# Optimization experiments

Measured on AMD Instinct MI355X. Metric: run time of the kernel, lower is better.

Reference implementation:

```python
import jax, jax.numpy as jnp
import numpy as np

B, L, H, NH = 4, 2048, 2048, 16
HD = H // NH  # head_dim = 128


def setup_inputs() -> dict:
    key = jax.random.key(0)
    ks = jax.random.split(key, 5)
    x = jax.random.normal(ks[0], (B, L, H), dtype=jnp.float32)
    Wqkv = jax.random.normal(ks[1], (H, 3 * H), dtype=jnp.float32) * (1.0 / np.sqrt(H))
    bqkv = jnp.zeros((3 * H,), dtype=jnp.float32)
    Wfc2 = jax.random.normal(ks[2], (H, H), dtype=jnp.float32) * (1.0 / np.sqrt(H))
    bfc2 = jnp.zeros((H,), dtype=jnp.float32)
    # RoPE tables over the FULL hidden dim (as in the torch module)
    inv_freq = 1.0 / (10000.0 ** (jnp.arange(0, H, 2, dtype=jnp.float32) / H))  # [H/2]
    t = jnp.arange(L, dtype=jnp.float32)
    freqs = jnp.outer(t, inv_freq)  # [L, H/2]
    return {"x": x, "Wqkv": Wqkv, "bqkv": bqkv, "Wfc2": Wfc2, "bfc2": bfc2,
            "cos": jnp.cos(freqs), "sin": jnp.sin(freqs)}


def _apply_rotary(u, cos, sin):
    # u: [b, l, H]; rotate halves over full hidden dim
    l = u.shape[1]
    d = u.shape[-1] // 2
    u1, u2 = u[..., :d], u[..., d:]
    c, s = cos[:l], sin[:l]  # [l, d] broadcast over batch
    return jnp.concatenate([u1 * c + u2 * s, -u1 * s + u2 * c], axis=-1)


def reference(x, Wqkv, bqkv, Wfc2, bfc2, cos, sin):
    b, l, _ = x.shape
    qkv = x @ Wqkv + bqkv  # [b, l, 3H]
    q, k, v = jnp.split(qkv, 3, axis=-1)
    q = _apply_rotary(q, cos, sin)
    k = _apply_rotary(k, cos, sin)
    # NOTE: heads are the FASTEST axis in the original view(b, l, head_dim, heads)
    def to_heads(u):
        return jnp.transpose(u.reshape(b, l, HD, NH), (0, 3, 1, 2))  # [b, h, l, d]
    q, k, v = to_heads(q), to_heads(k), to_heads(v)
    scale = 1.0 / np.sqrt(HD)
    scores = jnp.einsum('bhqd,bhkd->bhqk', q, k) * scale
    causal = jnp.tril(jnp.ones((l, l), dtype=bool))
    scores = jnp.where(causal, scores, jnp.finfo(scores.dtype).min)
    p = jax.nn.softmax(scores, axis=-1)
    y = jnp.einsum('bhqk,bhkd->bhqd', p, v)
    y = jnp.transpose(y, (0, 2, 1, 3)).reshape(b, l, H)  # [b, l, h*d]
    return jax.nn.silu(y @ Wfc2 + bfc2)
```

## Files before the change

### kernel.cpp

```cpp
#include <hip/hip_runtime.h>
#include <hip/hip_bf16.h>
#include <cstdint>
#include <cstddef>


typedef __attribute__((ext_vector_type(4))) float f32x4;
typedef __attribute__((ext_vector_type(8))) short bf16x8;
typedef __hip_bfloat16 bf16;

#define ASYNC16(lds, g)                                                                  \
  __builtin_amdgcn_global_load_lds((const __attribute__((address_space(1))) void*)(g),   \
                                   (__attribute__((address_space(3))) void*)(lds), 16, 0, 0)

__device__ __forceinline__ float b2f(bf16 v) { return __bfloat162float(v); }
__device__ __forceinline__ bf16 f2b(float v) { return __float2bfloat16(v); }
__device__ __forceinline__ short f2bs(float f) {
  bf16 h = __float2bfloat16(f);
  return __builtin_bit_cast(short, h);
}
__device__ __forceinline__ bf16x8 pack8(f32x4 a, f32x4 b) {
  bf16x8 r;
#pragma unroll
  for (int t = 0; t < 4; ++t) r[t] = f2bs(a[t]);
#pragma unroll
  for (int t = 0; t < 4; ++t) r[4 + t] = f2bs(b[t]);
  return r;
}

template <int CTRL>
__device__ __forceinline__ float dpp_bfly_max(float x) {
  int xi = __builtin_bit_cast(int, x);
  int yi = __builtin_amdgcn_update_dpp(xi, xi, CTRL, 0xF, 0xF, false);
  return fmaxf(x, __builtin_bit_cast(float, yi));
}
template <int CTRL>
__device__ __forceinline__ float dpp_bfly_add(float x) {
  int xi = __builtin_bit_cast(int, x);
  int yi = __builtin_amdgcn_update_dpp(xi, xi, CTRL, 0xF, 0xF, false);
  return x + __builtin_bit_cast(float, yi);
}

__global__ void conv_bf16(const float* __restrict__ src, bf16* __restrict__ dst) {
  size_t i = ((size_t)blockIdx.x * 256 + threadIdx.x) * 8;
  f32x4 a0 = *(const f32x4*)(src + i);
  f32x4 a1 = *(const f32x4*)(src + i + 4);
  *(bf16x8*)(dst + i) = pack8(a0, a1);
}

__global__ void transpose_conv(const float* __restrict__ src, bf16* __restrict__ dst,
                               int R, int C, int perm) {
  __shared__ float tile[32][33];
  int bx = blockIdx.x * 32, by = blockIdx.y * 32;
  int tx = threadIdx.x, ty = threadIdx.y;
  for (int i = ty; i < 32; i += 8) tile[i][tx] = src[(size_t)(by + i) * C + bx + tx];
  __syncthreads();
  for (int i = ty; i < 32; i += 8) {
    int c = bx + i;
    if (perm) {
      int cc = c & 2047;
      c = (c & ~2047) | (((cc & 15) << 7) | (cc >> 4));
    }
    dst[(size_t)c * R + by + tx] = f2b(tile[tx][i]);
  }
}

__global__ __launch_bounds__(256) void gemm_qkv(const bf16* __restrict__ A,
                                                const bf16* __restrict__ Bt,
                                                const float* __restrict__ biasf,
                                                bf16* __restrict__ Qg, bf16* __restrict__ Kg,
                                                bf16* __restrict__ Vg) {
  __shared__ alignas(16) bf16 smem[2 * 128 * 64];
  bf16* As = smem;
  bf16* Bs = smem + 128 * 64;
  const int K_ = 2048;
  int tid = threadIdx.x, lane = tid & 63, w = tid >> 6;
  int lr = lane & 15, hi = lane >> 4;
  int wm = (w >> 1) * 64, wn = (w & 1) * 64;
  int m0 = blockIdx.y * 128, n0 = blockIdx.x * 128;
  f32x4 acc[4][4];
#pragma unroll
  for (int im = 0; im < 4; ++im)
#pragma unroll
    for (int in = 0; in < 4; ++in) acc[im][in] = (f32x4){0.f, 0.f, 0.f, 0.f};

  for (int k0 = 0; k0 < K_; k0 += 64) {
    __syncthreads();
#pragma unroll
    for (int i = 0; i < 4; ++i) {
      int c = tid + 256 * i;
      int r = c >> 3, j = c & 7, jg = j ^ (r & 7);
      ASYNC16((char*)As + c * 16, (const char*)(A + (size_t)(m0 + r) * K_ + k0 + jg * 8));
    }
#pragma unroll
    for (int i = 0; i < 4; ++i) {
      int c = tid + 256 * i;
      int r = c >> 3, j = c & 7, jg = j ^ (r & 7);
      ASYNC16((char*)Bs + c * 16, (const char*)(Bt + (size_t)(n0 + r) * K_ + k0 + jg * 8));
    }
    __syncthreads();

#pragma unroll
    for (int ks = 0; ks < 2; ++ks) {
      bf16x8 afr[4], bfr[4];
#pragma unroll
      for (int im = 0; im < 4; ++im) {
        int r = wm + 16 * im + lr;
        afr[im] = *(const bf16x8*)((const char*)As + r * 128 + (((ks * 4 + hi) ^ (r & 7)) * 16));
      }
#pragma unroll
      for (int in = 0; in < 4; ++in) {
        int r = wn + 16 * in + lr;
        bfr[in] = *(const bf16x8*)((const char*)Bs + r * 128 + (((ks * 4 + hi) ^ (r & 7)) * 16));
      }
#pragma unroll
      for (int im = 0; im < 4; ++im)
#pragma unroll
        for (int in = 0; in < 4; ++in)
          acc[im][in] =
              __builtin_amdgcn_mfma_f32_16x16x32_bf16(afr[im], bfr[in], acc[im][in], 0, 0, 0);
    }
  }

  int which = n0 >> 11;
  int h = (n0 >> 7) & 15;
  int bq = m0 >> 11;
  int l_base = m0 & 2047;
  int bh = bq * 16 + h;
  float bv[4];
#pragma unroll
  for (int in = 0; in < 4; ++in)
    bv[in] = biasf[(which << 11) + ((wn + 16 * in + lr) << 4) + h];

  if (which < 2) {
    bf16* __restrict__ G = (which == 0) ? Qg : Kg;
#pragma unroll
    for (int im = 0; im < 4; ++im) {
#pragma unroll
      for (int in = 0; in < 4; ++in) {
        int d = wn + 16 * in + lr;
#pragma unroll
        for (int j = 0; j < 4; ++j) {
          int l = l_base + wm + 16 * im + 4 * hi + j;
          G[((size_t)bh * 2048 + l) * 128 + d] = f2b(acc[im][in][j] + bv[in]);
        }
      }
    }
  } else {
    __syncthreads();
#pragma unroll
    for (int im = 0; im < 4; ++im)
#pragma unroll
      for (int in = 0; in < 4; ++in) {
        int d = wn + 16 * in + lr;
#pragma unroll
        for (int j = 0; j < 4; ++j) {
          int l = wm + 16 * im + 4 * hi + j;
          int slot = (l >> 3) ^ (d & 15);
          smem[d * 128 + slot * 8 + (l & 7)] = f2b(acc[im][in][j] + bv[in]);
        }
      }
    __syncthreads();
#pragma unroll
    for (int s = 0; s < 8; ++s) {
      int d = (tid >> 4) + 16 * s;
      int lc = tid & 15;
      int slot = lc ^ (d & 15);
      bf16x8 v = *(const bf16x8*)(smem + d * 128 + slot * 8);
      *(bf16x8*)(Vg + ((size_t)bh * 128 + d) * 2048 + l_base + lc * 8) = v;
    }
  }
}

__global__ __launch_bounds__(256) void gemm_fc2(const bf16* __restrict__ A,
                                                const bf16* __restrict__ Bt,
                                                const float* __restrict__ biasf,
                                                float* __restrict__ Out) {
  __shared__ alignas(16) bf16 As[128 * 64];
  __shared__ alignas(16) bf16 Bs[128 * 64];
  const int K_ = 2048;
  int tid = threadIdx.x, lane = tid & 63, w = tid >> 6;
  int lr = lane & 15, hi = lane >> 4;
  int wm = (w >> 1) * 64, wn = (w & 1) * 64;
  int m0 = blockIdx.y * 128, n0 = blockIdx.x * 128;
  f32x4 acc[4][4];
#pragma unroll
  for (int im = 0; im < 4; ++im)
#pragma unroll
    for (int in = 0; in < 4; ++in) acc[im][in] = (f32x4){0.f, 0.f, 0.f, 0.f};

  for (int k0 = 0; k0 < K_; k0 += 64) {
    __syncthreads();
#pragma unroll
    for (int i = 0; i < 4; ++i) {
      int c = tid + 256 * i;
      int r = c >> 3, j = c & 7, jg = j ^ (r & 7);
      ASYNC16((char*)As + c * 16, (const char*)(A + (size_t)(m0 + r) * K_ + k0 + jg * 8));
    }
#pragma unroll
    for (int i = 0; i < 4; ++i) {
      int c = tid + 256 * i;
      int r = c >> 3, j = c & 7, jg = j ^ (r & 7);
      ASYNC16((char*)Bs + c * 16, (const char*)(Bt + (size_t)(n0 + r) * K_ + k0 + jg * 8));
    }
    __syncthreads();
#pragma unroll
    for (int ks = 0; ks < 2; ++ks) {
      bf16x8 afr[4], bfr[4];
#pragma unroll
      for (int im = 0; im < 4; ++im) {
        int r = wm + 16 * im + lr;
        afr[im] = *(const bf16x8*)((const char*)As + r * 128 + (((ks * 4 + hi) ^ (r & 7)) * 16));
      }
#pragma unroll
      for (int in = 0; in < 4; ++in) {
        int r = wn + 16 * in + lr;
        bfr[in] = *(const bf16x8*)((const char*)Bs + r * 128 + (((ks * 4 + hi) ^ (r & 7)) * 16));
      }
#pragma unroll
      for (int im = 0; im < 4; ++im)
#pragma unroll
        for (int in = 0; in < 4; ++in)
          acc[im][in] =
              __builtin_amdgcn_mfma_f32_16x16x32_bf16(afr[im], bfr[in], acc[im][in], 0, 0, 0);
    }
  }

#pragma unroll
  for (int im = 0; im < 4; ++im) {
#pragma unroll
    for (int in = 0; in < 4; ++in) {
      int c = n0 + wn + 16 * in + lr;
      float bv = biasf[c];
#pragma unroll
      for (int j = 0; j < 4; ++j) {
        int m = m0 + wm + 16 * im + 4 * hi + j;
        float z = acc[im][in][j] + bv;
        Out[(size_t)m * 2048 + c] = z / (1.f + __expf(-z));
      }
    }
  }
}

__global__ void rotary_kernel(bf16* __restrict__ Qg, bf16* __restrict__ Kg,
                              const float* __restrict__ cosp, const float* __restrict__ sinp) {
  int idx = blockIdx.x * 256 + threadIdx.x;
  int d = idx & 63;
  int l = (idx >> 6) & 2047;
  int bh = idx >> 17;
  int h = bh & 15;
  size_t base = ((size_t)bh * 2048 + l) * 128;
  int ang = l * 1024 + d * 16 + h;
  float c = cosp[ang], s = sinp[ang];
  float q1 = b2f(Qg[base + d]), q2 = b2f(Qg[base + d + 64]);
  Qg[base + d] = f2b(q1 * c + q2 * s);
  Qg[base + d + 64] = f2b(-q1 * s + q2 * c);
  float k1 = b2f(Kg[base + d]), k2 = b2f(Kg[base + d + 64]);
  Kg[base + d] = f2b(k1 * c + k2 * s);
  Kg[base + d + 64] = f2b(-k1 * s + k2 * c);
}

__global__ __launch_bounds__(512) void flash_kernel(const bf16* __restrict__ Qg,
                                                    const bf16* __restrict__ Kg,
                                                    const bf16* __restrict__ Vg,
                                                    bf16* __restrict__ Y) {
  __shared__ alignas(16) bf16 Ks[64 * 128];
  __shared__ alignas(16) bf16 Vt[128 * 64];
  __shared__ alignas(16) bf16 Ps[8 * 16 * 72];
  int tid = threadIdx.x, lane = tid & 63, w = tid >> 6;
  int lr = lane & 15, hi = lane >> 4;
  int it = 15 - (int)blockIdx.x;
  int bh = blockIdx.y;
  int b = bh >> 4, h = bh & 15;
  int q0 = it * 128;
  int qb = q0 + 16 * w;
  const bf16* Qb = Qg + (size_t)bh * 2048 * 128;
  const bf16* Kb = Kg + (size_t)bh * 2048 * 128;
  const bf16* Vb = Vg + (size_t)bh * 128 * 2048;
  const float NEG = -1.0e30f;

  bf16x8 qf[4];
#pragma unroll
  for (int ks = 0; ks < 4; ++ks)
    qf[ks] = *(const bf16x8*)(Qb + (size_t)(qb + lr) * 128 + (ks * 4 + hi) * 8);

  bf16x8 kreg[2], vreg[2];
#pragma unroll
  for (int i = 0; i < 2; ++i) {
    int c = tid + 512 * i;
    int rk = c >> 4, jk = (c & 15) ^ (rk & 7);
    kreg[i] = *(const bf16x8*)(Kb + (size_t)rk * 128 + jk * 8);
    int rv = c >> 3, jv = (c & 7) ^ (rv & 7);
    vreg[i] = *(const bf16x8*)(Vb + (size_t)rv * 2048 + jv * 8);
  }

  f32x4 o[8];
#pragma unroll
  for (int i = 0; i < 8; ++i) o[i] = (f32x4){0.f, 0.f, 0.f, 0.f};
  float m_i[4], l_i[4];
#pragma unroll
  for (int j = 0; j < 4; ++j) { m_i[j] = NEG; l_i[j] = 0.f; }
  const float scale = 0.08838834764831845f;

  int jt_max = 2 * it + 1;
  for (int jt = 0; jt <= jt_max; ++jt) {
    int k0 = jt * 64;
    __syncthreads();
#pragma unroll
    for (int i = 0; i < 2; ++i) {
      int c = tid + 512 * i;
      *(bf16x8*)((char*)Ks + c * 16) = kreg[i];
      *(bf16x8*)((char*)Vt + c * 16) = vreg[i];
    }
    __syncthreads();

    if (jt < jt_max) {
      int k0n = k0 + 64;
#pragma unroll
      for (int i = 0; i < 2; ++i) {
        int c = tid + 512 * i;
        int rk = c >> 4, jk = (c & 15) ^ (rk & 7);
        kreg[i] = *(const bf16x8*)(Kb + (size_t)(k0n + rk) * 128 + jk * 8);
        int rv = c >> 3, jv = (c & 7) ^ (rv & 7);
        vreg[i] = *(const bf16x8*)(Vb + (size_t)rv * 2048 + k0n + jv * 8);
      }
    }

    if (k0 > qb + 15) continue;

    f32x4 sacc[4];
#pragma unroll
    for (int in = 0; in < 4; ++in) sacc[in] = (f32x4){0.f, 0.f, 0.f, 0.f};
#pragma unroll
    for (int ks = 0; ks < 4; ++ks) {
#pragma unroll
      for (int in = 0; in < 4; ++in) {
        int br = 16 * in + lr;
        bf16x8 bb =
            *(const bf16x8*)((const char*)Ks + br * 256 + (((ks * 4 + hi) ^ (br & 7)) * 16));
        sacc[in] = __builtin_amdgcn_mfma_f32_16x16x32_bf16(qf[ks], bb, sacc[in], 0, 0, 0);
      }
    }

    bool needmask = (k0 + 63 > qb);
    float mxr[4], alpha[4], rsum[4];
#pragma unroll
    for (int j = 0; j < 4; ++j) {
      float mx = NEG;
#pragma unroll
      for (int in = 0; in < 4; ++in) {
        float s = sacc[in][j] * scale;
        if (needmask) {
          int qg_ = qb + 4 * hi + j;
          int kg_ = k0 + 16 * in + lr;
          if (kg_ > qg_) s = NEG;
        }
        sacc[in][j] = s;
        mx = fmaxf(mx, s);
      }
      mxr[j] = mx;
    }
#pragma unroll
    for (int j = 0; j < 4; ++j) mxr[j] = dpp_bfly_max<0xB1>(mxr[j]);
#pragma unroll
    for (int j = 0; j < 4; ++j) mxr[j] = dpp_bfly_max<0x4E>(mxr[j]);
#pragma unroll
    for (int j = 0; j < 4; ++j) mxr[j] = dpp_bfly_max<0x141>(mxr[j]);
#pragma unroll
    for (int j = 0; j < 4; ++j) mxr[j] = dpp_bfly_max<0x140>(mxr[j]);

#pragma unroll
    for (int j = 0; j < 4; ++j) {
      float mnew = fmaxf(m_i[j], mxr[j]);
      alpha[j] = __expf(m_i[j] - mnew);
      m_i[j] = mnew;
      float r = 0.f;
#pragma unroll
      for (int in = 0; in < 4; ++in) {
        float p = __expf(sacc[in][j] - mnew);
        sacc[in][j] = p;
        r += p;
      }
      rsum[j] = r;
    }
#pragma unroll
    for (int j = 0; j < 4; ++j) rsum[j] = dpp_bfly_add<0xB1>(rsum[j]);
#pragma unroll
    for (int j = 0; j < 4; ++j) rsum[j] = dpp_bfly_add<0x4E>(rsum[j]);
#pragma unroll
    for (int j = 0; j < 4; ++j) rsum[j] = dpp_bfly_add<0x141>(rsum[j]);
#pragma unroll
    for (int j = 0; j < 4; ++j) rsum[j] = dpp_bfly_add<0x140>(rsum[j]);

#pragma unroll
    for (int j = 0; j < 4; ++j) {
      l_i[j] = alpha[j] * l_i[j] + rsum[j];
#pragma unroll
      for (int inp = 0; inp < 8; ++inp) o[inp][j] *= alpha[j];
    }

#pragma unroll
    for (int j = 0; j < 4; ++j)
#pragma unroll
      for (int in = 0; in < 4; ++in)
        Ps[w * 1152 + (4 * hi + j) * 72 + 16 * in + lr] = f2b(sacc[in][j]);
    asm volatile("s_waitcnt lgkmcnt(0)" ::: "memory");

#pragma unroll
    for (int ko = 0; ko < 2; ++ko) {
      bf16x8 a = *(const bf16x8*)((const char*)Ps + (w * 1152 + lr * 72 + ko * 32 + hi * 8) * 2);
#pragma unroll
      for (int inp = 0; inp < 8; ++inp) {
        int br = 16 * inp + lr;
        bf16x8 bb =
            *(const bf16x8*)((const char*)Vt + br * 128 + (((ko * 4 + hi) ^ (br & 7)) * 16));
        o[inp] = __builtin_amdgcn_mfma_f32_16x16x32_bf16(a, bb, o[inp], 0, 0, 0);
      }
    }
  }

#pragma unroll
  for (int j = 0; j < 4; ++j) {
    int qg_ = qb + 4 * hi + j;
    float inv = 1.f / l_i[j];
    size_t rowb = ((size_t)(b * 2048 + qg_)) * 2048 + h * 128;
#pragma unroll
    for (int inp = 0; inp < 8; ++inp) {
      int dd = 16 * inp + lr;
      Y[rowb + dd] = f2b(o[inp][j] * inv);
    }
  }
}

extern "C" void kernel_launch(void* const* d_in, const int* in_sizes, int n_in,
                              void* d_out, int out_size, void* d_ws, size_t ws_size,
                              hipStream_t stream) {
  const float* x    = (const float*)d_in[0];
  const float* Wqkv = (const float*)d_in[1];
  const float* bqkv = (const float*)d_in[2];
  const float* Wfc2 = (const float*)d_in[3];
  const float* bfc2 = (const float*)d_in[4];
  const float* cosp = (const float*)d_in[5];
  const float* sinp = (const float*)d_in[6];
  float* out = (float*)d_out;

  bf16* ws = (bf16*)d_ws;
  bf16* Yg    = ws;
  bf16* WqkvT = ws;
  bf16* Qg    = ws + 16777216;
  bf16* Wfc2T = ws + 16777216;
  bf16* Kg    = ws + 33554432;
  bf16* Vg    = ws + 50331648;
  bf16* xb    = (bf16*)d_out;

  conv_bf16<<<8192, 256, 0, stream>>>(x, xb);
  transpose_conv<<<dim3(192, 64), dim3(32, 8), 0, stream>>>(Wqkv, WqkvT, 2048, 6144, 1);
  gemm_qkv<<<dim3(48, 64), 256, 0, stream>>>(xb, WqkvT, bqkv, Qg, Kg, Vg);
  rotary_kernel<<<32768, 256, 0, stream>>>(Qg, Kg, cosp, sinp);
  flash_kernel<<<dim3(16, 64), 512, 0, stream>>>(Qg, Kg, Vg, Yg);
  transpose_conv<<<dim3(64, 64), dim3(32, 8), 0, stream>>>(Wfc2, Wfc2T, 2048, 2048, 0);
  gemm_fc2<<<dim3(16, 64), 256, 0, stream>>>(Yg, Wfc2T, bfc2, out);
}
```

Baseline: 801.3 us.

## Fuse rotary into QKV epilogue and flash Q load; add lazy softmax rescale

Drops the standalone rotary kernel. RoPE on K now runs in the QKV GEMM epilogue through an LDS-staged, swizzled row layout, and RoPE on Q is applied to the Q fragments in registers when the flash kernel loads them. This removes a full read-modify-write pass over Q and K. The flash kernel also skips the running-max update and the output rescale when every row's new max stays within 8 of the old one (a wave-wide vote), and the row-sum reductions are reordered after the P stores. The cost is extra cos/sin gathers inside both kernels and somewhat larger unnormalised exponentials when the rescale is skipped.

```diff
diff --git a/kernel.cpp b/kernel.cpp
--- a/kernel.cpp
+++ b/kernel.cpp
@@ -17,6 +17,9 @@
 __device__ __forceinline__ short f2bs(float f) {
   bf16 h = __float2bfloat16(f);
   return __builtin_bit_cast(short, h);
+}
+__device__ __forceinline__ float s2f(short s) {
+  return __bfloat162float(__builtin_bit_cast(bf16, s));
 }
 __device__ __forceinline__ bf16x8 pack8(f32x4 a, f32x4 b) {
   bf16x8 r;
@@ -67,6 +70,8 @@
 __global__ __launch_bounds__(256) void gemm_qkv(const bf16* __restrict__ A,
                                                 const bf16* __restrict__ Bt,
                                                 const float* __restrict__ biasf,
+                                                const float* __restrict__ cosp,
+                                                const float* __restrict__ sinp,
                                                 bf16* __restrict__ Qg, bf16* __restrict__ Kg,
                                                 bf16* __restrict__ Vg) {
   __shared__ alignas(16) bf16 smem[2 * 128 * 64];
@@ -131,8 +136,7 @@
   for (int in = 0; in < 4; ++in)
     bv[in] = biasf[(which << 11) + ((wn + 16 * in + lr) << 4) + h];
 
-  if (which < 2) {
-    bf16* __restrict__ G = (which == 0) ? Qg : Kg;
+  if (which == 0) {
 #pragma unroll
     for (int im = 0; im < 4; ++im) {
 #pragma unroll
@@ -141,9 +145,46 @@
 #pragma unroll
         for (int j = 0; j < 4; ++j) {
           int l = l_base + wm + 16 * im + 4 * hi + j;
-          G[((size_t)bh * 2048 + l) * 128 + d] = f2b(acc[im][in][j] + bv[in]);
+          Qg[((size_t)bh * 2048 + l) * 128 + d] = f2b(acc[im][in][j] + bv[in]);
         }
       }
+    }
+  } else if (which == 1) {
+    __syncthreads();
+#pragma unroll
+    for (int im = 0; im < 4; ++im)
+#pragma unroll
+      for (int in = 0; in < 4; ++in) {
+        int d = wn + 16 * in + lr;
+#pragma unroll
+        for (int j = 0; j < 4; ++j) {
+          int lw = wm + 16 * im + 4 * hi + j;
+          smem[lw * 128 + (((d >> 3) ^ (lw & 15)) << 3) + (d & 7)] =
+              f2b(acc[im][in][j] + bv[in]);
+        }
+      }
+    __syncthreads();
+#pragma unroll
+    for (int t = 0; t < 4; ++t) {
+      int g = tid + 256 * t;
+      int lw = g >> 3, c = g & 7;
+      bf16x8 v1 = *(const bf16x8*)(smem + lw * 128 + ((c ^ (lw & 15)) << 3));
+      bf16x8 v2 = *(const bf16x8*)(smem + lw * 128 + (((c + 8) ^ (lw & 15)) << 3));
+      int l = l_base + lw;
+      size_t abase = (size_t)l * 1024 + h;
+      bf16x8 r1, r2;
+#pragma unroll
+      for (int e = 0; e < 8; ++e) {
+        int dd = c * 8 + e;
+        float cv = cosp[abase + dd * 16];
+        float sv = sinp[abase + dd * 16];
+        float k1 = s2f(v1[e]), k2 = s2f(v2[e]);
+        r1[e] = f2bs(k1 * cv + k2 * sv);
+        r2[e] = f2bs(-k1 * sv + k2 * cv);
+      }
+      bf16* Kr = Kg + ((size_t)bh * 2048 + l) * 128;
+      *(bf16x8*)(Kr + c * 8) = r1;
+      *(bf16x8*)(Kr + c * 8 + 64) = r2;
     }
   } else {
     __syncthreads();
@@ -241,27 +282,11 @@
   }
 }
 
-__global__ void rotary_kernel(bf16* __restrict__ Qg, bf16* __restrict__ Kg,
-                              const float* __restrict__ cosp, const float* __restrict__ sinp) {
-  int idx = blockIdx.x * 256 + threadIdx.x;
-  int d = idx & 63;
-  int l = (idx >> 6) & 2047;
-  int bh = idx >> 17;
-  int h = bh & 15;
-  size_t base = ((size_t)bh * 2048 + l) * 128;
-  int ang = l * 1024 + d * 16 + h;
-  float c = cosp[ang], s = sinp[ang];
-  float q1 = b2f(Qg[base + d]), q2 = b2f(Qg[base + d + 64]);
-  Qg[base + d] = f2b(q1 * c + q2 * s);
-  Qg[base + d + 64] = f2b(-q1 * s + q2 * c);
-  float k1 = b2f(Kg[base + d]), k2 = b2f(Kg[base + d + 64]);
-  Kg[base + d] = f2b(k1 * c + k2 * s);
-  Kg[base + d + 64] = f2b(-k1 * s + k2 * c);
-}
-
 __global__ __launch_bounds__(512) void flash_kernel(const bf16* __restrict__ Qg,
                                                     const bf16* __restrict__ Kg,
                                                     const bf16* __restrict__ Vg,
+                                                    const float* __restrict__ cosp,
+                                                    const float* __restrict__ sinp,
                                                     bf16* __restrict__ Y) {
   __shared__ alignas(16) bf16 Ks[64 * 128];
   __shared__ alignas(16) bf16 Vt[128 * 64];
@@ -282,6 +307,20 @@
 #pragma unroll
   for (int ks = 0; ks < 4; ++ks)
     qf[ks] = *(const bf16x8*)(Qb + (size_t)(qb + lr) * 128 + (ks * 4 + hi) * 8);
+  {
+    size_t arow = (size_t)(qb + lr) * 1024 + h;
+#pragma unroll
+    for (int ks = 0; ks < 2; ++ks)
+#pragma unroll
+      for (int e = 0; e < 8; ++e) {
+        int dd = 32 * ks + 8 * hi + e;
+        float cv = cosp[arow + dd * 16];
+        float sv = sinp[arow + dd * 16];
+        float q1 = s2f(qf[ks][e]), q2 = s2f(qf[ks + 2][e]);
+        qf[ks][e] = f2bs(q1 * cv + q2 * sv);
+        qf[ks + 2][e] = f2bs(-q1 * sv + q2 * cv);
+      }
+  }
 
   bf16x8 kreg[2], vreg[2];
 #pragma unroll
@@ -342,7 +381,7 @@
     }
 
     bool needmask = (k0 + 63 > qb);
-    float mxr[4], alpha[4], rsum[4];
+    float mxr[4];
 #pragma unroll
     for (int j = 0; j < 4; ++j) {
       float mx = NEG;
@@ -368,41 +407,56 @@
 #pragma unroll
     for (int j = 0; j < 4; ++j) mxr[j] = dpp_bfly_max<0x140>(mxr[j]);
 
+    int okc = 1;
+#pragma unroll
+    for (int j = 0; j < 4; ++j) okc &= (mxr[j] <= m_i[j] + 8.f) ? 1 : 0;
+    bool skip = __all(okc);
+    float mnew[4];
+#pragma unroll
+    for (int j = 0; j < 4; ++j) mnew[j] = skip ? m_i[j] : fmaxf(m_i[j], mxr[j]);
+
+    float rsum[4];
 #pragma unroll
     for (int j = 0; j < 4; ++j) {
-      float mnew = fmaxf(m_i[j], mxr[j]);
-      alpha[j] = __expf(m_i[j] - mnew);
-      m_i[j] = mnew;
       float r = 0.f;
 #pragma unroll
       for (int in = 0; in < 4; ++in) {
-        float p = __expf(sacc[in][j] - mnew);
+        float p = __expf(sacc[in][j] - mnew[j]);
         sacc[in][j] = p;
         r += p;
       }
       rsum[j] = r;
     }
-#pragma unroll
-    for (int j = 0; j < 4; ++j) rsum[j] = dpp_bfly_add<0xB1>(rsum[j]);
-#pragma unroll
-    for (int j = 0; j < 4; ++j) rsum[j] = dpp_bfly_add<0x4E>(rsum[j]);
-#pragma unroll
-    for (int j = 0; j < 4; ++j) rsum[j] = dpp_bfly_add<0x141>(rsum[j]);
-#pragma unroll
-    for (int j = 0; j < 4; ++j) rsum[j] = dpp_bfly_add<0x140>(rsum[j]);
-
-#pragma unroll
-    for (int j = 0; j < 4; ++j) {
-      l_i[j] = alpha[j] * l_i[j] + rsum[j];
-#pragma unroll
-      for (int inp = 0; inp < 8; ++inp) o[inp][j] *= alpha[j];
-    }
 
 #pragma unroll
     for (int j = 0; j < 4; ++j)
 #pragma unroll
       for (int in = 0; in < 4; ++in)
         Ps[w * 1152 + (4 * hi + j) * 72 + 16 * in + lr] = f2b(sacc[in][j]);
+
+#pragma unroll
+    for (int j = 0; j < 4; ++j) rsum[j] = dpp_bfly_add<0xB1>(rsum[j]);
+#pragma unroll
+    for (int j = 0; j < 4; ++j) rsum[j] = dpp_bfly_add<0x4E>(rsum[j]);
+#pragma unroll
+    for (int j = 0; j < 4; ++j) rsum[j] = dpp_bfly_add<0x141>(rsum[j]);
+#pragma unroll
+    for (int j = 0; j < 4; ++j) rsum[j] = dpp_bfly_add<0x140>(rsum[j]);
+
+    if (skip) {
+#pragma unroll
+      for (int j = 0; j < 4; ++j) l_i[j] += rsum[j];
+    } else {
+#pragma unroll
+      for (int j = 0; j < 4; ++j) {
+        float alpha = __expf(m_i[j] - mnew[j]);
+        m_i[j] = mnew[j];
+        l_i[j] = alpha * l_i[j] + rsum[j];
+#pragma unroll
+        for (int inp = 0; inp < 8; ++inp) o[inp][j] *= alpha;
+      }
+    }
+
     asm volatile("s_waitcnt lgkmcnt(0)" ::: "memory");
 
 #pragma unroll
@@ -454,9 +508,8 @@
 
   conv_bf16<<<8192, 256, 0, stream>>>(x, xb);
   transpose_conv<<<dim3(192, 64), dim3(32, 8), 0, stream>>>(Wqkv, WqkvT, 2048, 6144, 1);
-  gemm_qkv<<<dim3(48, 64), 256, 0, stream>>>(xb, WqkvT, bqkv, Qg, Kg, Vg);
-  rotary_kernel<<<32768, 256, 0, stream>>>(Qg, Kg, cosp, sinp);
-  flash_kernel<<<dim3(16, 64), 512, 0, stream>>>(Qg, Kg, Vg, Yg);
+  gemm_qkv<<<dim3(48, 64), 256, 0, stream>>>(xb, WqkvT, bqkv, cosp, sinp, Qg, Kg, Vg);
+  flash_kernel<<<dim3(16, 64), 512, 0, stream>>>(Qg, Kg, Vg, cosp, sinp, Yg);
   transpose_conv<<<dim3(64, 64), dim3(32, 8), 0, stream>>>(Wfc2, Wfc2T, 2048, 2048, 0);
   gemm_fc2<<<dim3(16, 64), 256, 0, stream>>>(Yg, Wfc2T, bfc2, out);
 }
```

Result: slower. 964.8 us (+20.4%).
